# Kernel optimization log

Measured on AMD Instinct MI355X. Metric: run time of the kernel, lower is better.

## Reference

```python
import jax, jax.numpy as jnp
import numpy as np

B, IN, U = 4096, 256, 128
G, LW, LB = 1000, 64, 32


def setup_inputs() -> dict:
    key = jax.random.key(0)
    ks = jax.random.split(key, 9)
    return {
        "x": jax.random.normal(ks[0], (B, IN), dtype=jnp.float32),
        "eps_w": jax.random.normal(ks[1], (B, LW), dtype=jnp.float32),
        "eps_b": jax.random.normal(ks[2], (B, LB), dtype=jnp.float32),
        "zw_mu": jax.random.normal(ks[3], (G, LW), dtype=jnp.float32) * 0.05,
        "zw_sigma": jax.random.normal(ks[4], (G, LW), dtype=jnp.float32),
        "Wf": jax.random.normal(ks[5], (LW, IN * U), dtype=jnp.float32) * (1.0 / np.sqrt(LW)),
        "zb_mu": jnp.zeros((G, LB), dtype=jnp.float32),
        "zb_sigma": jax.random.normal(ks[6], (G, LB), dtype=jnp.float32),
        "Bf": jax.random.normal(ks[7], (LB, U), dtype=jnp.float32) * (1.0 / np.sqrt(LB)),
        "gid": jax.random.randint(ks[8], (B,), 0, G, dtype=jnp.int32),
    }


def reference(x, eps_w, eps_b, zw_mu, zw_sigma, Wf, zb_mu, zb_sigma, Bf, gid):
    # --- multilevel weights: gather group posterior, reparameterized sample ---
    mu_w = zw_mu[gid]                                  # [B, LW]
    sig_w = jax.nn.softplus(zw_sigma[gid])             # [B, LW]
    zw_samp = mu_w + sig_w * eps_w                     # [B, LW]
    w = (zw_samp @ Wf).reshape(B, IN, U)               # factor out to per-example weights
    # --- multilevel bias ---
    mu_b = zb_mu[gid]                                  # [B, LB]
    sig_b = jax.nn.softplus(zb_sigma[gid])             # [B, LB]
    b = (mu_b + sig_b * eps_b) @ Bf                    # [B, U]
    # --- batched per-example matmul: w^T @ x  (tf.matmul(w, x, transpose_a=True)) ---
    out = jnp.einsum("bi,biu->bu", x, w) + b           # [B, U]
    return out  # activation is None (linear)
```

## Files before the change

### kernel.cpp

```cpp
#include <hip/hip_runtime.h>
#include <hip/hip_bf16.h>
#include <stdint.h>

#define B_SZ   4096
#define IN_SZ  256
#define U_SZ   128
#define G_SZ   1000
#define LW_SZ  64
#define LB_SZ  32
#define K_SZ   (LW_SZ * IN_SZ)

#define BM     128
#define BK     64
#define KSPL   16
#define NSTEP  16
#define NTILE  (K_SZ / BK)
#define CHUNK  (BK * U_SZ)

typedef __attribute__((ext_vector_type(8))) short  bf16x8;
typedef __attribute__((ext_vector_type(4))) float  f32x4;
typedef __attribute__((ext_vector_type(8))) _Float16 f16x8;
typedef __attribute__((ext_vector_type(2))) _Float16 f16x2;
typedef __attribute__((ext_vector_type(4))) _Float16 f16x4;

typedef const void __attribute__((address_space(1)))* gas_ptr;
typedef void __attribute__((address_space(3)))* las_ptr;

__device__ __forceinline__ ushort f2bf(float f) {
    unsigned u = __float_as_uint(f);
    u += 0x7fffu + ((u >> 16) & 1u);
    return (ushort)(u >> 16);
}

__device__ __forceinline__ float softplus_f(float v) {
    return fmaxf(v, 0.0f) + log1pf(__expf(-fabsf(v)));
}

__global__ __launch_bounds__(256) void fmd_prep(
    const float* __restrict__ Wf, const float* __restrict__ x,
    short* __restrict__ wfT, short* __restrict__ xh)
{
    const int tid = threadIdx.x;
    if (blockIdx.x < NTILE) {
        const int t = blockIdx.x;
        __shared__ float lds[64 * 132];
        #pragma unroll
        for (int it = 0; it < 8; ++it) {
            int idx = it * 256 + tid;
            int kk = idx >> 5, u4 = idx & 31;
            float4 v = *reinterpret_cast<const float4*>(&Wf[(t * 64 + kk) * U_SZ + u4 * 4]);
            *reinterpret_cast<float4*>(&lds[kk * 132 + u4 * 4]) = v;
        }
        __syncthreads();
        short* chunk = wfT + t * CHUNK;
        #pragma unroll
        for (int g = 0; g < 4; ++g) {
            int p = g * 2048 + tid * 8;
            int u = p >> 6;
            int cc = p & 63;
            int kk0 = cc ^ ((u & 7) << 3);
            union { _Float16 h[8]; f16x8 v; } pk;
            #pragma unroll
            for (int j = 0; j < 8; ++j)
                pk.h[j] = (_Float16)lds[(kk0 + j) * 132 + u];
            *reinterpret_cast<f16x8*>(&chunk[p]) = pk.v;
        }
    } else {
        const int bb = blockIdx.x - NTILE;
        const int mt = bb >> 2, c = bb & 3;
        short* chunk = xh + bb * CHUNK;
        #pragma unroll
        for (int g = 0; g < 4; ++g) {
            int p = g * 2048 + tid * 8;
            int r = p >> 6;
            int cc0 = (p & 63) ^ ((r & 7) << 3);
            const float* src = &x[(mt * BM + r) * IN_SZ + c * 64 + cc0];
            float4 a = *reinterpret_cast<const float4*>(src);
            float4 b = *reinterpret_cast<const float4*>(src + 4);
            union { _Float16 h[8]; f16x8 v; } pk;
            pk.h[0] = (_Float16)a.x; pk.h[1] = (_Float16)a.y;
            pk.h[2] = (_Float16)a.z; pk.h[3] = (_Float16)a.w;
            pk.h[4] = (_Float16)b.x; pk.h[5] = (_Float16)b.y;
            pk.h[6] = (_Float16)b.z; pk.h[7] = (_Float16)b.w;
            *reinterpret_cast<f16x8*>(&chunk[p]) = pk.v;
        }
    }
}

__global__ __launch_bounds__(256, 2) void fmd_gemm3(
    const short* __restrict__ xh,
    const short* __restrict__ wfT,
    const float* __restrict__ zw_mu,
    const float* __restrict__ zw_sigma,
    const float* __restrict__ eps_w,
    const int*   __restrict__ gid,
    _Float16*    __restrict__ part)
{
    const int tid  = threadIdx.x;
    const int lane = tid & 63;
    const int wid  = tid >> 6;
    const int wr   = wid >> 1;
    const int wc   = wid & 1;
    const int bid  = blockIdx.x;
    const int ks   = bid & (KSPL - 1);
    const int mt   = bid >> 4;
    const int m0   = mt * BM;

    __shared__ short As[2][CHUNK];
    __shared__ short Bs[2][CHUNK];

    f16x2 zwp[4][4];
    #pragma unroll
    for (int m = 0; m < 4; ++m) {
        int row = wr * 64 + m * 16 + (lane & 15);
        int b   = m0 + row;
        int g   = gid[b];
        float4 mu = *reinterpret_cast<const float4*>(&zw_mu[g * LW_SZ + ks * 4]);
        float4 sg = *reinterpret_cast<const float4*>(&zw_sigma[g * LW_SZ + ks * 4]);
        float4 ep = *reinterpret_cast<const float4*>(&eps_w[b * LW_SZ + ks * 4]);
        float v0 = mu.x + softplus_f(sg.x) * ep.x;
        float v1 = mu.y + softplus_f(sg.y) * ep.y;
        float v2 = mu.z + softplus_f(sg.z) * ep.z;
        float v3 = mu.w + softplus_f(sg.w) * ep.w;
        _Float16 h0 = (_Float16)v0, h1 = (_Float16)v1, h2 = (_Float16)v2, h3 = (_Float16)v3;
        zwp[m][0] = (f16x2){h0, h0};
        zwp[m][1] = (f16x2){h1, h1};
        zwp[m][2] = (f16x2){h2, h2};
        zwp[m][3] = (f16x2){h3, h3};
    }

    const int soff = wid * 2048 + lane * 8;
    const int doff = wid * 2048;

    {
        const short* sA = xh + (mt * 4 + 0) * CHUNK;
        const short* sB = wfT + (ks * 16 + 0) * CHUNK;
        #pragma unroll
        for (int j = 0; j < 4; ++j) {
            __builtin_amdgcn_global_load_lds((gas_ptr)(sA + soff + j * 512),
                                             (las_ptr)(&As[0][doff + j * 512]), 16, 0, 0);
            __builtin_amdgcn_global_load_lds((gas_ptr)(sB + soff + j * 512),
                                             (las_ptr)(&Bs[0][doff + j * 512]), 16, 0, 0);
        }
    }
    __syncthreads();

    f32x4 acc[4][4];
    #pragma unroll
    for (int m = 0; m < 4; ++m)
        #pragma unroll
        for (int n = 0; n < 4; ++n)
            acc[m][n] = (f32x4){0.f, 0.f, 0.f, 0.f};

    for (int c = 0; c < 4; ++c) {
        #pragma unroll
        for (int li = 0; li < 4; ++li) {
            const int s = c * 4 + li;
            if (s < NSTEP - 1) {
                const int sn = s + 1, cn = sn >> 2, lin = sn & 3;
                const short* sB = wfT + (ks * 16 + lin * 4 + cn) * CHUNK;
                short* dB = &Bs[sn & 1][doff];
                #pragma unroll
                for (int j = 0; j < 4; ++j)
                    __builtin_amdgcn_global_load_lds((gas_ptr)(sB + soff + j * 512),
                                                     (las_ptr)(dB + j * 512), 16, 0, 0);
                if (lin == 0) {
                    const short* sA = xh + (mt * 4 + cn) * CHUNK;
                    short* dA = &As[cn & 1][doff];
                    #pragma unroll
                    for (int j = 0; j < 4; ++j)
                        __builtin_amdgcn_global_load_lds((gas_ptr)(sA + soff + j * 512),
                                                         (las_ptr)(dA + j * 512), 16, 0, 0);
                }
            }
            __builtin_amdgcn_sched_barrier(0);

            const short* Ab = As[c & 1];
            const short* Bb = Bs[s & 1];
            #pragma unroll
            for (int kb = 0; kb < 2; ++kb) {
                union { f16x8 v8; f16x2 v2[4]; } af[4], bfv[4], as_[4];
                #pragma unroll
                for (int m = 0; m < 4; ++m) {
                    int row = wr * 64 + m * 16 + (lane & 15);
                    int si = (row * BK + kb * 32 + (lane >> 4) * 8) ^ ((row & 7) << 3);
                    af[m].v8 = *reinterpret_cast<const f16x8*>(&Ab[si]);
                }
                #pragma unroll
                for (int n = 0; n < 4; ++n) {
                    int rowu = wc * 64 + n * 16 + (lane & 15);
                    int si = (rowu * BK + kb * 32 + (lane >> 4) * 8) ^ ((rowu & 7) << 3);
                    bfv[n].v8 = *reinterpret_cast<const f16x8*>(&Bb[si]);
                }
                #pragma unroll
                for (int m = 0; m < 4; ++m) {
                    #pragma unroll
                    for (int w = 0; w < 4; ++w)
                        as_[m].v2[w] = af[m].v2[w] * zwp[m][li];
                }
                #pragma unroll
                for (int m = 0; m < 4; ++m)
                    #pragma unroll
                    for (int n = 0; n < 4; ++n)
                        acc[m][n] = __builtin_amdgcn_mfma_f32_16x16x32_f16(
                            as_[m].v8, bfv[n].v8, acc[m][n], 0, 0, 0);
            }
            __syncthreads();
        }
    }

    _Float16* dst = part + (size_t)ks * (B_SZ * U_SZ);
    #pragma unroll
    for (int m = 0; m < 4; ++m) {
        int row0 = m0 + wr * 64 + m * 16 + ((lane >> 4) << 2);
        #pragma unroll
        for (int n = 0; n < 4; ++n) {
            int col = wc * 64 + n * 16 + (lane & 15);
            #pragma unroll
            for (int j = 0; j < 4; ++j)
                dst[(row0 + j) * U_SZ + col] = (_Float16)acc[m][n][j];
        }
    }
}

__global__ __launch_bounds__(256) void fmd_reduce2(
    const _Float16* __restrict__ part,
    const float* __restrict__ eps_b,
    const float* __restrict__ zb_mu,
    const float* __restrict__ zb_sigma,
    const float* __restrict__ Bf,
    const int*   __restrict__ gid,
    float*       __restrict__ out)
{
    const int tid = threadIdx.x;
    const int bid = blockIdx.x;
    const int i   = bid * 256 + tid;
    const int bl  = tid >> 5;
    const int u4  = tid & 31;

    __shared__ float zb[8][33];
    {
        int b2 = bid * 8 + bl;
        int g  = gid[b2];
        float sg = softplus_f(zb_sigma[g * LB_SZ + u4]);
        zb[bl][u4] = zb_mu[g * LB_SZ + u4] + sg * eps_b[b2 * LB_SZ + u4];
    }
    __syncthreads();

    const f32x4* Bf4 = (const f32x4*)Bf;
    f32x4 acc = (f32x4){0.f, 0.f, 0.f, 0.f};
    #pragma unroll
    for (int l = 0; l < LB_SZ; ++l)
        acc += zb[bl][l] * Bf4[l * 32 + u4];

    #pragma unroll
    for (int ks = 0; ks < KSPL; ++ks) {
        f16x4 p = *reinterpret_cast<const f16x4*>(&part[(size_t)ks * (B_SZ * U_SZ) + (size_t)i * 4]);
        acc[0] += (float)p[0];
        acc[1] += (float)p[1];
        acc[2] += (float)p[2];
        acc[3] += (float)p[3];
    }
    ((f32x4*)out)[i] = acc;
}

__global__ __launch_bounds__(256) void fmd_bias(
    const float* __restrict__ eps_b,
    const float* __restrict__ zb_mu,
    const float* __restrict__ zb_sigma,
    const float* __restrict__ Bf,
    const int*   __restrict__ gid,
    float*       __restrict__ out)
{
    const int half = threadIdx.x >> 7;
    const int u    = threadIdx.x & 127;
    const int b    = blockIdx.x * 2 + half;

    __shared__ float zb[2][LB_SZ];
    if (u < LB_SZ) {
        int g = gid[b];
        float sg = softplus_f(zb_sigma[g * LB_SZ + u]);
        zb[half][u] = zb_mu[g * LB_SZ + u] + sg * eps_b[b * LB_SZ + u];
    }
    __syncthreads();

    float acc = 0.0f;
    #pragma unroll
    for (int l = 0; l < LB_SZ; ++l)
        acc += zb[half][l] * Bf[l * U_SZ + u];
    out[b * U_SZ + u] = acc;
}

__global__ __launch_bounds__(256, 2) void fmd_gemm_legacy(
    const float* __restrict__ x,
    const float* __restrict__ eps_w,
    const float* __restrict__ zw_mu,
    const float* __restrict__ zw_sigma,
    const float* __restrict__ Wf,
    const int*   __restrict__ gid,
    float*       __restrict__ out)
{
    const int tid  = threadIdx.x;
    const int lane = tid & 63;
    const int wid  = tid >> 6;
    const int wr   = wid >> 1;
    const int wc   = wid & 1;
    const int bid  = blockIdx.x;
    const int ks   = bid & (KSPL - 1);
    const int mt   = bid >> 4;
    const int m0   = mt * BM;

    __shared__ short As[BM * BK];
    __shared__ short Bs[U_SZ * BK];
    __shared__ float zw_s[BM][4];

    for (int it = tid; it < BM * 4; it += 256) {
        int r = it >> 2, lloc = it & 3;
        int b = m0 + r;
        int g = gid[b];
        int l = ks * 4 + lloc;
        float sg = softplus_f(zw_sigma[g * LW_SZ + l]);
        zw_s[r][lloc] = zw_mu[g * LW_SZ + l] + sg * eps_w[b * LW_SZ + l];
    }

    f32x4 acc[4][4];
    #pragma unroll
    for (int m = 0; m < 4; ++m)
        #pragma unroll
        for (int n = 0; n < 4; ++n)
            acc[m][n] = (f32x4){0.f, 0.f, 0.f, 0.f};

    for (int s = 0; s < NSTEP; ++s) {
        __syncthreads();
        const int li = s >> 2;
        const int i0 = (s & 3) * BK;
        const int k0 = ks * (K_SZ / KSPL) + s * BK;

        #pragma unroll
        for (int it = 0; it < 8; ++it) {
            int idx = it * 256 + tid;
            int r = idx >> 4, c4 = idx & 15;
            float4 xv = *reinterpret_cast<const float4*>(&x[(m0 + r) * IN_SZ + i0 + c4 * 4]);
            float zw = zw_s[r][li];
            ushort h0 = f2bf(xv.x * zw), h1 = f2bf(xv.y * zw);
            ushort h2 = f2bf(xv.z * zw), h3 = f2bf(xv.w * zw);
            unsigned long long pw = (unsigned long long)h0
                                  | ((unsigned long long)h1 << 16)
                                  | ((unsigned long long)h2 << 32)
                                  | ((unsigned long long)h3 << 48);
            int si = (r * BK + c4 * 4) ^ ((r & 7) << 3);
            *reinterpret_cast<unsigned long long*>(&As[si]) = pw;
        }
        #pragma unroll
        for (int it = 0; it < 4; ++it) {
            int idx = it * 256 + tid;
            int u = idx & 127, kg = idx >> 7;
            union { ushort h[8]; bf16x8 v; } pk;
            #pragma unroll
            for (int j = 0; j < 8; ++j)
                pk.h[j] = f2bf(Wf[(k0 + kg * 8 + j) * U_SZ + u]);
            int si = (u * BK + kg * 8) ^ ((u & 7) << 3);
            *reinterpret_cast<bf16x8*>(&Bs[si]) = pk.v;
        }
        __syncthreads();

        #pragma unroll
        for (int kb = 0; kb < 2; ++kb) {
            bf16x8 af[4], bfr[4];
            #pragma unroll
            for (int m = 0; m < 4; ++m) {
                int row = wr * 64 + m * 16 + (lane & 15);
                int si = (row * BK + kb * 32 + (lane >> 4) * 8) ^ ((row & 7) << 3);
                af[m] = *reinterpret_cast<const bf16x8*>(&As[si]);
            }
            #pragma unroll
            for (int n = 0; n < 4; ++n) {
                int rowu = wc * 64 + n * 16 + (lane & 15);
                int si = (rowu * BK + kb * 32 + (lane >> 4) * 8) ^ ((rowu & 7) << 3);
                bfr[n] = *reinterpret_cast<const bf16x8*>(&Bs[si]);
            }
            #pragma unroll
            for (int m = 0; m < 4; ++m)
                #pragma unroll
                for (int n = 0; n < 4; ++n)
                    acc[m][n] = __builtin_amdgcn_mfma_f32_16x16x32_bf16(af[m], bfr[n], acc[m][n], 0, 0, 0);
        }
    }

    #pragma unroll
    for (int m = 0; m < 4; ++m) {
        int row0 = m0 + wr * 64 + m * 16 + ((lane >> 4) << 2);
        #pragma unroll
        for (int n = 0; n < 4; ++n) {
            int col = wc * 64 + n * 16 + (lane & 15);
            #pragma unroll
            for (int j = 0; j < 4; ++j)
                atomicAdd(&out[(row0 + j) * U_SZ + col], acc[m][n][j]);
        }
    }
}

extern "C" void kernel_launch(void* const* d_in, const int* in_sizes, int n_in,
                              void* d_out, int out_size, void* d_ws, size_t ws_size,
                              hipStream_t stream) {
    const float* x        = (const float*)d_in[0];
    const float* eps_w    = (const float*)d_in[1];
    const float* eps_b    = (const float*)d_in[2];
    const float* zw_mu    = (const float*)d_in[3];
    const float* zw_sigma = (const float*)d_in[4];
    const float* Wf       = (const float*)d_in[5];
    const float* zb_mu    = (const float*)d_in[6];
    const float* zb_sigma = (const float*)d_in[7];
    const float* Bf       = (const float*)d_in[8];
    const int*   gid      = (const int*)d_in[9];
    float* out = (float*)d_out;

    const size_t WFT_BYTES  = (size_t)K_SZ * U_SZ * 2;
    const size_t XH_OFF     = WFT_BYTES;
    const size_t XH_BYTES   = (size_t)B_SZ * IN_SZ * 2;
    const size_t PART_OFF   = XH_OFF + XH_BYTES;
    const size_t PART_BYTES = (size_t)KSPL * B_SZ * U_SZ * 2;

    if (ws_size >= PART_OFF + PART_BYTES) {
        short*     wfT  = (short*)d_ws;
        short*     xh   = (short*)((char*)d_ws + XH_OFF);
        _Float16*  part = (_Float16*)((char*)d_ws + PART_OFF);
        fmd_prep<<<NTILE + (B_SZ / BM) * 4, 256, 0, stream>>>(Wf, x, wfT, xh);
        fmd_gemm3<<<(B_SZ / BM) * KSPL, 256, 0, stream>>>(
            xh, wfT, zw_mu, zw_sigma, eps_w, gid, part);
        fmd_reduce2<<<(B_SZ * U_SZ) / 1024, 256, 0, stream>>>(
            part, eps_b, zb_mu, zb_sigma, Bf, gid, out);
    } else {
        fmd_bias<<<B_SZ / 2, 256, 0, stream>>>(eps_b, zb_mu, zb_sigma, Bf, gid, out);
        fmd_gemm_legacy<<<(B_SZ / BM) * KSPL, 256, 0, stream>>>(
            x, eps_w, zw_mu, zw_sigma, Wf, gid, out);
    }
}
```

Measured before the change: 43.96 us.

## Triple-buffer B tiles with prefetch distance two and fine-grained vmcnt waits

The GEMM main loop moves from double to triple buffering of the weight tiles. It prefetches two steps ahead and loads the x tile earlier, in the middle of each chunk. Full __syncthreads are replaced by explicit s_waitcnt vmcnt(N) plus s_barrier, so later loads can stay in flight while the current tile is consumed, and MFMA sections are raised in priority with s_setprio. This is meant to hide global-to-LDS latency better, at the cost of more LDS per block and fragile hand-counted wait thresholds.

```diff
diff --git a/kernel.cpp b/kernel.cpp
--- a/kernel.cpp
+++ b/kernel.cpp
@@ -87,7 +87,7 @@
     }
 }
 
-__global__ __launch_bounds__(256, 2) void fmd_gemm3(
+__global__ __launch_bounds__(256, 2) void fmd_gemm4(
     const short* __restrict__ xh,
     const short* __restrict__ wfT,
     const float* __restrict__ zw_mu,
@@ -107,7 +107,7 @@
     const int m0   = mt * BM;
 
     __shared__ short As[2][CHUNK];
-    __shared__ short Bs[2][CHUNK];
+    __shared__ short Bs[3][CHUNK];
 
     f16x2 zwp[4][4];
     #pragma unroll
@@ -133,17 +133,24 @@
     const int doff = wid * 2048;
 
     {
-        const short* sA = xh + (mt * 4 + 0) * CHUNK;
-        const short* sB = wfT + (ks * 16 + 0) * CHUNK;
-        #pragma unroll
-        for (int j = 0; j < 4; ++j) {
-            __builtin_amdgcn_global_load_lds((gas_ptr)(sA + soff + j * 512),
+        const short* sB0 = wfT + (ks * 16 + 0) * CHUNK;
+        const short* sA0 = xh + (mt * 4 + 0) * CHUNK;
+        const short* sB1 = wfT + (ks * 16 + 4) * CHUNK;
+        #pragma unroll
+        for (int j = 0; j < 4; ++j)
+            __builtin_amdgcn_global_load_lds((gas_ptr)(sB0 + soff + j * 512),
+                                             (las_ptr)(&Bs[0][doff + j * 512]), 16, 0, 0);
+        #pragma unroll
+        for (int j = 0; j < 4; ++j)
+            __builtin_amdgcn_global_load_lds((gas_ptr)(sA0 + soff + j * 512),
                                              (las_ptr)(&As[0][doff + j * 512]), 16, 0, 0);
-            __builtin_amdgcn_global_load_lds((gas_ptr)(sB + soff + j * 512),
-                                             (las_ptr)(&Bs[0][doff + j * 512]), 16, 0, 0);
-        }
-    }
-    __syncthreads();
+        #pragma unroll
+        for (int j = 0; j < 4; ++j)
+            __builtin_amdgcn_global_load_lds((gas_ptr)(sB1 + soff + j * 512),
+                                             (las_ptr)(&Bs[1][doff + j * 512]), 16, 0, 0);
+    }
+    asm volatile("s_waitcnt vmcnt(4)" ::: "memory");
+    __builtin_amdgcn_s_barrier();
 
     f32x4 acc[4][4];
     #pragma unroll
@@ -152,60 +159,73 @@
         for (int n = 0; n < 4; ++n)
             acc[m][n] = (f32x4){0.f, 0.f, 0.f, 0.f};
 
-    for (int c = 0; c < 4; ++c) {
-        #pragma unroll
-        for (int li = 0; li < 4; ++li) {
-            const int s = c * 4 + li;
-            if (s < NSTEP - 1) {
-                const int sn = s + 1, cn = sn >> 2, lin = sn & 3;
-                const short* sB = wfT + (ks * 16 + lin * 4 + cn) * CHUNK;
-                short* dB = &Bs[sn & 1][doff];
+    #pragma unroll
+    for (int s = 0; s < NSTEP; ++s) {
+        const int c  = s >> 2;
+        const int li = s & 3;
+
+        if (s + 2 < NSTEP) {
+            const int s2 = s + 2;
+            const short* sB = wfT + (ks * 16 + (s2 & 3) * 4 + (s2 >> 2)) * CHUNK;
+            short* dB = &Bs[s2 % 3][doff];
+            #pragma unroll
+            for (int j = 0; j < 4; ++j)
+                __builtin_amdgcn_global_load_lds((gas_ptr)(sB + soff + j * 512),
+                                                 (las_ptr)(dB + j * 512), 16, 0, 0);
+        }
+        if (li == 2 && c < 3) {
+            const short* sA = xh + (mt * 4 + c + 1) * CHUNK;
+            short* dA = &As[(c + 1) & 1][doff];
+            #pragma unroll
+            for (int j = 0; j < 4; ++j)
+                __builtin_amdgcn_global_load_lds((gas_ptr)(sA + soff + j * 512),
+                                                 (las_ptr)(dA + j * 512), 16, 0, 0);
+        }
+        __builtin_amdgcn_sched_barrier(0);
+
+        const short* Ab = As[c & 1];
+        const short* Bb = Bs[s % 3];
+        __builtin_amdgcn_s_setprio(1);
+        #pragma unroll
+        for (int kb = 0; kb < 2; ++kb) {
+            union { f16x8 v8; f16x2 v2[4]; } af[4], bfv[4], as_[4];
+            #pragma unroll
+            for (int m = 0; m < 4; ++m) {
+                int row = wr * 64 + m * 16 + (lane & 15);
+                int si = (row * BK + kb * 32 + (lane >> 4) * 8) ^ ((row & 7) << 3);
+                af[m].v8 = *reinterpret_cast<const f16x8*>(&Ab[si]);
+            }
+            #pragma unroll
+            for (int n = 0; n < 4; ++n) {
+                int rowu = wc * 64 + n * 16 + (lane & 15);
+                int si = (rowu * BK + kb * 32 + (lane >> 4) * 8) ^ ((rowu & 7) << 3);
+                bfv[n].v8 = *reinterpret_cast<const f16x8*>(&Bb[si]);
+            }
+            #pragma unroll
+            for (int m = 0; m < 4; ++m) {
                 #pragma unroll
-                for (int j = 0; j < 4; ++j)
-                    __builtin_amdgcn_global_load_lds((gas_ptr)(sB + soff + j * 512),
-                                                     (las_ptr)(dB + j * 512), 16, 0, 0);
-                if (lin == 0) {
-                    const short* sA = xh + (mt * 4 + cn) * CHUNK;
-                    short* dA = &As[cn & 1][doff];
-                    #pragma unroll
-                    for (int j = 0; j < 4; ++j)
-                        __builtin_amdgcn_global_load_lds((gas_ptr)(sA + soff + j * 512),
-                                                         (las_ptr)(dA + j * 512), 16, 0, 0);
-                }
+                for (int w = 0; w < 4; ++w)
+                    as_[m].v2[w] = af[m].v2[w] * zwp[m][li];
             }
-            __builtin_amdgcn_sched_barrier(0);
-
-            const short* Ab = As[c & 1];
-            const short* Bb = Bs[s & 1];
-            #pragma unroll
-            for (int kb = 0; kb < 2; ++kb) {
-                union { f16x8 v8; f16x2 v2[4]; } af[4], bfv[4], as_[4];
+            #pragma unroll
+            for (int m = 0; m < 4; ++m)
                 #pragma unroll
-                for (int m = 0; m < 4; ++m) {
-                    int row = wr * 64 + m * 16 + (lane & 15);
-                    int si = (row * BK + kb * 32 + (lane >> 4) * 8) ^ ((row & 7) << 3);
-                    af[m].v8 = *reinterpret_cast<const f16x8*>(&Ab[si]);
-                }
-                #pragma unroll
-                for (int n = 0; n < 4; ++n) {
-                    int rowu = wc * 64 + n * 16 + (lane & 15);
-                    int si = (rowu * BK + kb * 32 + (lane >> 4) * 8) ^ ((rowu & 7) << 3);
-                    bfv[n].v8 = *reinterpret_cast<const f16x8*>(&Bb[si]);
-                }
-                #pragma unroll
-                for (int m = 0; m < 4; ++m) {
-                    #pragma unroll
-                    for (int w = 0; w < 4; ++w)
-                        as_[m].v2[w] = af[m].v2[w] * zwp[m][li];
-                }
-                #pragma unroll
-                for (int m = 0; m < 4; ++m)
-                    #pragma unroll
-                    for (int n = 0; n < 4; ++n)
-                        acc[m][n] = __builtin_amdgcn_mfma_f32_16x16x32_f16(
-                            as_[m].v8, bfv[n].v8, acc[m][n], 0, 0, 0);
-            }
-            __syncthreads();
+                for (int n = 0; n < 4; ++n)
+                    acc[m][n] = __builtin_amdgcn_mfma_f32_16x16x32_f16(
+                        as_[m].v8, bfv[n].v8, acc[m][n], 0, 0, 0);
+        }
+        __builtin_amdgcn_s_setprio(0);
+
+        if (s == 14) {
+            asm volatile("s_waitcnt vmcnt(0) lgkmcnt(0)" ::: "memory");
+            __builtin_amdgcn_s_barrier();
+        } else if (s == 15) {
+        } else if (li == 2) {
+            asm volatile("s_waitcnt vmcnt(8) lgkmcnt(0)" ::: "memory");
+            __builtin_amdgcn_s_barrier();
+        } else {
+            asm volatile("s_waitcnt vmcnt(4) lgkmcnt(0)" ::: "memory");
+            __builtin_amdgcn_s_barrier();
         }
     }
 
@@ -426,7 +446,7 @@
         short*     xh   = (short*)((char*)d_ws + XH_OFF);
         _Float16*  part = (_Float16*)((char*)d_ws + PART_OFF);
         fmd_prep<<<NTILE + (B_SZ / BM) * 4, 256, 0, stream>>>(Wf, x, wfT, xh);
-        fmd_gemm3<<<(B_SZ / BM) * KSPL, 256, 0, stream>>>(
+        fmd_gemm4<<<(B_SZ / BM) * KSPL, 256, 0, stream>>>(
             xh, wfT, zw_mu, zw_sigma, eps_w, gid, part);
         fmd_reduce2<<<(B_SZ * U_SZ) / 1024, 256, 0, stream>>>(
             part, eps_b, zb_mu, zb_sigma, Bf, gid, out);
```

Result: no change. 44.55 us (+1.4%).
